# Kernel optimization log

Measured on AMD Instinct MI355X. Metric: run time of the kernel, lower is better.

The kernel has to match this reference:

```python
import jax, jax.numpy as jnp
import numpy as np

MODEL_DIM = 2048
NUM_HEADS = 32
HEAD_DIM = 64
NUM_KV_HEADS = 8
ROPE_BASE = 10000.0
BATCH = 2
SEQ = 2048


def setup_inputs() -> dict:
    key = jax.random.key(0)
    ks = jax.random.split(key, 5)
    sd = 1.0 / np.sqrt(MODEL_DIM)
    x = jax.random.normal(ks[0], (BATCH, SEQ, MODEL_DIM), dtype=jnp.float32)
    Wq = jax.random.normal(ks[1], (MODEL_DIM, NUM_HEADS * HEAD_DIM), dtype=jnp.float32) * sd
    Wk = jax.random.normal(ks[2], (MODEL_DIM, NUM_KV_HEADS * HEAD_DIM), dtype=jnp.float32) * sd
    Wv = jax.random.normal(ks[3], (MODEL_DIM, NUM_KV_HEADS * HEAD_DIM), dtype=jnp.float32) * sd
    Wo = jax.random.normal(ks[4], (NUM_HEADS * HEAD_DIM, MODEL_DIM), dtype=jnp.float32) * sd
    return {"x": x, "Wq": Wq, "Wk": Wk, "Wv": Wv, "Wo": Wo}


def _rope_cache(seq_len, head_dim, base, dtype):
    # inv_freq over even dims, standard rotate-half (Llama-style) RoPE cache
    inv_freq = 1.0 / (base ** (jnp.arange(0, head_dim, 2, dtype=jnp.float32) / head_dim))
    t = jnp.arange(seq_len, dtype=jnp.float32)
    freqs = jnp.outer(t, inv_freq)               # [S, hd/2]
    emb = jnp.concatenate([freqs, freqs], axis=-1)  # [S, hd]
    return jnp.cos(emb).astype(dtype), jnp.sin(emb).astype(dtype)


def _rotate_half(x):
    h = x.shape[-1] // 2
    return jnp.concatenate([-x[..., h:], x[..., :h]], axis=-1)


def _apply_rope(q, k, cos, sin):
    # q,k: [B, H, S, hd]; cos,sin: [S, hd] -> broadcast over batch/heads
    cos = cos[None, None, :, :]
    sin = sin[None, None, :, :]
    q = q * cos + _rotate_half(q) * sin
    k = k * cos + _rotate_half(k) * sin
    return q, k


def reference(x, Wq, Wk, Wv, Wo):
    bsz, seq_len, _ = x.shape
    q_per_kv = NUM_HEADS // NUM_KV_HEADS

    # projections -> [B, H, S, hd]
    q = (x @ Wq).reshape(bsz, seq_len, NUM_HEADS, HEAD_DIM).transpose(0, 2, 1, 3)
    k = (x @ Wk).reshape(bsz, seq_len, NUM_KV_HEADS, HEAD_DIM).transpose(0, 2, 1, 3)
    v = (x @ Wv).reshape(bsz, seq_len, NUM_KV_HEADS, HEAD_DIM).transpose(0, 2, 1, 3)

    # GQA: repeat_interleave KV heads to match Q heads
    k = jnp.repeat(k, q_per_kv, axis=1)
    v = jnp.repeat(v, q_per_kv, axis=1)

    cos, sin = _rope_cache(seq_len, HEAD_DIM, ROPE_BASE, x.dtype)
    q, k = _apply_rope(q, k, cos, sin)

    scale = 1.0 / np.sqrt(HEAD_DIM)
    scores = jnp.einsum('bhqd,bhkd->bhqk', q, k) * scale  # [B,H,S,S]
    causal = jnp.tril(jnp.ones((seq_len, seq_len), dtype=bool))
    scores = jnp.where(causal[None, None], scores, jnp.finfo(scores.dtype).min)
    attn = jax.nn.softmax(scores, axis=-1)
    y = jnp.einsum('bhqk,bhkd->bhqd', attn, v)  # [B,H,S,hd]

    y = y.transpose(0, 2, 1, 3).reshape(bsz, seq_len, NUM_HEADS * HEAD_DIM)
    return y @ Wo
```

## Files before the change

kernel.cpp:

```cpp
#include <hip/hip_runtime.h>
#include <cstdint>

typedef unsigned short u16;
typedef __attribute__((ext_vector_type(8))) short short8;
typedef __attribute__((ext_vector_type(4))) short short4v;
typedef __attribute__((ext_vector_type(4))) float f32x4;

#define SEQ     2048
#define NHEADS  32
#define NKV     8
#define HD      64
#define DM      2048
#define MROWS   4096
#define KVSTR   1024
#define PSTR    88

__device__ __forceinline__ float b2f(unsigned int u) {
    return __builtin_bit_cast(float, u << 16);
}
__device__ __forceinline__ u16 f2b(float f) {
    unsigned int u = __builtin_bit_cast(unsigned int, f);
    return (u16)((u + 0x7fffu + ((u >> 16) & 1u)) >> 16);
}

__device__ __forceinline__ float dpp_red_max16(float x) {
    int v = __builtin_bit_cast(int, x);
    x = fmaxf(x, __builtin_bit_cast(float,
        __builtin_amdgcn_update_dpp(v, v, 0xB1, 0xF, 0xF, true)));
    v = __builtin_bit_cast(int, x);
    x = fmaxf(x, __builtin_bit_cast(float,
        __builtin_amdgcn_update_dpp(v, v, 0x4E, 0xF, 0xF, true)));
    v = __builtin_bit_cast(int, x);
    x = fmaxf(x, __builtin_bit_cast(float,
        __builtin_amdgcn_update_dpp(v, v, 0x141, 0xF, 0xF, true)));
    v = __builtin_bit_cast(int, x);
    x = fmaxf(x, __builtin_bit_cast(float,
        __builtin_amdgcn_update_dpp(v, v, 0x140, 0xF, 0xF, true)));
    return x;
}
__device__ __forceinline__ float dpp_red_sum16(float x) {
    int v = __builtin_bit_cast(int, x);
    x = x + __builtin_bit_cast(float,
        __builtin_amdgcn_update_dpp(v, v, 0xB1, 0xF, 0xF, true));
    v = __builtin_bit_cast(int, x);
    x = x + __builtin_bit_cast(float,
        __builtin_amdgcn_update_dpp(v, v, 0x4E, 0xF, 0xF, true));
    v = __builtin_bit_cast(int, x);
    x = x + __builtin_bit_cast(float,
        __builtin_amdgcn_update_dpp(v, v, 0x141, 0xF, 0xF, true));
    v = __builtin_bit_cast(int, x);
    x = x + __builtin_bit_cast(float,
        __builtin_amdgcn_update_dpp(v, v, 0x140, 0xF, 0xF, true));
    return x;
}

#define GLOAD_LDS16(g, l)                                              \
    __builtin_amdgcn_global_load_lds(                                  \
        (const __attribute__((address_space(1))) void*)(g),            \
        (__attribute__((address_space(3))) void*)(l), 16, 0, 0)

__global__ __launch_bounds__(256) void cvt_f32_bf16(
    const float* __restrict__ in, u16* __restrict__ out, int n4) {
    int i = blockIdx.x * 256 + threadIdx.x;
    if (i < n4) {
        float4 v = ((const float4*)in)[i];
        ushort4 o;
        o.x = f2b(v.x); o.y = f2b(v.y); o.z = f2b(v.z); o.w = f2b(v.w);
        ((ushort4*)out)[i] = o;
    }
}

__global__ __launch_bounds__(256) void rope_table_kernel(
    float* __restrict__ cosT, float* __restrict__ sinT) {
    int idx = blockIdx.x * 256 + threadIdx.x;
    int s  = idx >> 5;
    int dl = idx & 31;
    float inv_freq = exp2f((float)dl * -0.41524101186092025f);
    float ang = (float)s * inv_freq;
    float sn, cs;
    sincosf(ang, &sn, &cs);
    cosT[idx] = cs;
    sinT[idx] = sn;
}

__global__ __launch_bounds__(256) void transpose_f32_bf16(
    const float* __restrict__ in, u16* __restrict__ out, int K, int N) {
    __shared__ float tile[32][33];
    int n0 = blockIdx.x * 32, k0 = blockIdx.y * 32;
    int tx = threadIdx.x, ty = threadIdx.y;
    for (int r = ty; r < 32; r += 8)
        tile[r][tx] = in[(size_t)(k0 + r) * N + n0 + tx];
    __syncthreads();
    for (int r = ty; r < 32; r += 8)
        out[(size_t)(n0 + r) * K + k0 + tx] = f2b(tile[tx][r]);
}

#define GEMM_BODY(Aptr, BTptr, Kdim)                                        \
    __shared__ __align__(16) u16 rA[3][4096];                               \
    __shared__ __align__(16) u16 rB[3][4096];                               \
    const int tid  = threadIdx.x;                                           \
    const int wid  = tid >> 6;                                              \
    const int lane = tid & 63;                                              \
    const int quad = lane >> 4;                                             \
    const int l16  = lane & 15;                                             \
    const int nwg  = gridDim.x * gridDim.y;                                 \
    const int fid  = blockIdx.y * gridDim.x + blockIdx.x;                   \
    const int swz  = (fid & 7) * (nwg >> 3) + (fid >> 3);                   \
    const int rowBase = (swz / gridDim.x) * 128;                            \
    const int colBase = (swz % gridDim.x) * 128;                            \
    const int wr = (wid >> 1) * 64;                                         \
    const int wc = (wid & 1) * 64;                                          \
    size_t sAoff[2], sBoff[2];                                              \
    int ldOff[2];                                                           \
    _Pragma("unroll")                                                       \
    for (int j = 0; j < 2; ++j) {                                           \
        const int p = j * 256 + tid;       \
        const int q = p >> 3;                                               \
        const int u = (p & 7) ^ (q & 7);               \
        const int r = (q << 1) | (u >> 2);                                  \
        const int sc = (u & 3) * 8;              \
        sAoff[j] = (size_t)(rowBase + r) * (Kdim) + sc;                     \
        sBoff[j] = (size_t)(colBase + r) * (Kdim) + sc;                     \
        ldOff[j] = (j * 256 + (wid << 6)) * 8;    \
    }                                                                       \
    int aOff[4], bOff[4];                  \
    _Pragma("unroll")                                                       \
    for (int mi = 0; mi < 4; ++mi) {                                        \
        const int ra = wr + mi * 16 + l16;                                  \
        const int qa = ra >> 1;                                             \
        const int ua = ((ra & 1) << 2) | quad;                              \
        aOff[mi] = (qa * 8 + (ua ^ (qa & 7))) * 8;                          \
        const int rb = wc + mi * 16 + l16;                                  \
        const int qb = rb >> 1;                                             \
        const int ub = ((rb & 1) << 2) | quad;                              \
        bOff[mi] = (qb * 8 + (ub ^ (qb & 7))) * 8;                          \
    }                                                                       \
    f32x4 acc[4][4] = {};                                                   \
    const int NT = (Kdim) / 32;                                             \
    _Pragma("unroll")                                                       \
    for (int st = 0; st < 3; ++st) {       \
        _Pragma("unroll")                                                   \
        for (int j = 0; j < 2; ++j) {                                       \
            GLOAD_LDS16(Aptr  + sAoff[j] + st * 32, &rA[st][ldOff[j]]);     \
            GLOAD_LDS16(BTptr + sBoff[j] + st * 32, &rB[st][ldOff[j]]);     \
        }                                                                   \
    }                                                                       \
    int bs = 0;                            \
    for (int s = 0; s < NT; ++s) {                                          \
        if (s < NT - 1)                                                     \
            asm volatile("s_waitcnt vmcnt(4)\n\ts_barrier" ::: "memory");   \
        else                                                                \
            asm volatile("s_waitcnt vmcnt(0)\n\ts_barrier" ::: "memory");   \
        const u16* Ab = rA[bs];                                             \
        const u16* Bb = rB[bs];                                             \
        short8 a[4], b[4];                                                  \
        _Pragma("unroll")                                                   \
        for (int mi = 0; mi < 4; ++mi) a[mi] = *(const short8*)&Ab[aOff[mi]]; \
        _Pragma("unroll")                                                   \
        for (int ni = 0; ni < 4; ++ni) b[ni] = *(const short8*)&Bb[bOff[ni]]; \
        if (s + 2 < NT) {                           \
            const int bi = bs == 0 ? 2 : bs - 1;               \
            const int kk = (s + 2) * 32;                                    \
            _Pragma("unroll")                                               \
            for (int j = 0; j < 2; ++j) {                                   \
                GLOAD_LDS16(Aptr  + sAoff[j] + kk, &rA[bi][ldOff[j]]);      \
                GLOAD_LDS16(BTptr + sBoff[j] + kk, &rB[bi][ldOff[j]]);      \
            }                                                               \
        }                                                                   \
        __builtin_amdgcn_s_setprio(1);                                      \
        _Pragma("unroll")                                                   \
        for (int mi = 0; mi < 4; ++mi)                                      \
            _Pragma("unroll")                                               \
            for (int ni = 0; ni < 4; ++ni)                                  \
                acc[mi][ni] = __builtin_amdgcn_mfma_f32_16x16x32_bf16(      \
                    a[mi], b[ni], acc[mi][ni], 0, 0, 0);                    \
        __builtin_amdgcn_s_setprio(0);                                      \
        bs = bs == 2 ? 0 : bs + 1;                                          \
    }                                                                       \
    const int wRow = rowBase + wr;                                          \
    const int wCol = colBase + wc;

__global__ __launch_bounds__(256, 3) void gemm_qkv(
    const u16* __restrict__ A, const u16* __restrict__ BT,
    u16* __restrict__ Qb, u16* __restrict__ KVb,
    const float* __restrict__ cosT, const float* __restrict__ sinT) {
    GEMM_BODY(A, BT, DM)

    u16* dst;
    int dstride, dcol;
    float scale;
    bool doRope;
    if (wCol < 2048)      { dst = Qb;  dstride = 2048; dcol = wCol;        scale = 0.125f; doRope = true;  }
    else if (wCol < 2560) { dst = KVb; dstride = 1024; dcol = wCol - 2048; scale = 1.0f;   doRope = true;  }
    else                  { dst = KVb; dstride = 1024; dcol = wCol - 2048; scale = 1.0f;   doRope = false; }

#pragma unroll
    for (int mi = 0; mi < 4; ++mi) {
#pragma unroll
        for (int r = 0; r < 4; ++r) {
            const int R = wRow + mi * 16 + quad * 4 + r;
            u16* crow = dst + (size_t)R * dstride + dcol;
            if (doRope) {
                const int s = R & (SEQ - 1);
#pragma unroll
                for (int ni = 0; ni < 2; ++ni) {
                    const int dl = ni * 16 + l16;
                    float lo = acc[mi][ni][r];
                    float hi = acc[mi][ni + 2][r];
                    float cs = cosT[s * 32 + dl];
                    float sn = sinT[s * 32 + dl];
                    crow[dl]      = f2b((lo * cs - hi * sn) * scale);
                    crow[dl + 32] = f2b((hi * cs + lo * sn) * scale);
                }
            } else {
#pragma unroll
                for (int ni = 0; ni < 4; ++ni)
                    crow[ni * 16 + l16] = f2b(acc[mi][ni][r]);
            }
        }
    }
}

__global__ __launch_bounds__(256, 3) void gemm_out(
    const u16* __restrict__ A, const u16* __restrict__ BT,
    float* __restrict__ C32) {
    GEMM_BODY(A, BT, DM)
#pragma unroll
    for (int mi = 0; mi < 4; ++mi) {
#pragma unroll
        for (int r = 0; r < 4; ++r) {
            const int R = wRow + mi * 16 + quad * 4 + r;
            float* crow = C32 + (size_t)R * DM + wCol;
#pragma unroll
            for (int ni = 0; ni < 4; ++ni)
                crow[ni * 16 + l16] = acc[mi][ni][r];
        }
    }
}

__global__ __launch_bounds__(512, 4) void flash_attn(
    const u16* __restrict__ Q, const u16* __restrict__ KV,
    u16* __restrict__ Yb, float* __restrict__ PoA,
    float* __restrict__ Ml) {
    __shared__ __align__(16) u16 Ks[64 * 64];
    __shared__ __align__(16) u16 Vt[64 * 72];
    __shared__ __align__(16) u16 Ps[8 * 16 * PSTR];

    const int p   = blockIdx.x >> 1;
    const int sh  = blockIdx.x & 1;
    const int h   = blockIdx.y;
    const int b   = blockIdx.z;
    const int kvh = h >> 2;
    const int tid  = threadIdx.x;
    const int wid  = tid >> 6;
    const int lane = tid & 63;
    const int quad = lane >> 4;
    const int l16  = lane & 15;

    const u16* Kg = KV + (size_t)b * SEQ * KVSTR + kvh * HD;
    const u16* Vg = Kg + 512;
    u16* Psw = Ps + wid * 16 * PSTR;

    const int kKey = tid >> 3, kCc = tid & 7;
    const int vkp  = tid & 31;
    const int vd0  = (tid >> 5) * 4;

    for (int ph = 0; ph < 2; ++ph) {
        const int qt = ph ? (15 - p) : p;
        const int hc = ph ? (16 - p) : (p + 1);
        const int tS = sh * hc;
        const int rowBaseW = qt * 128 + wid * 16;

        short8 qf[2];
#pragma unroll
        for (int ks = 0; ks < 2; ++ks)
            qf[ks] = *(const short8*)&Q[
                (size_t)(b * SEQ + rowBaseW + l16) * (NHEADS * HD)
                + h * HD + ks * 32 + quad * 8];

        f32x4 o[4] = {};
        float mi[4], li[4];
#pragma unroll
        for (int r = 0; r < 4; ++r) { mi[r] = -3e38f; li[r] = 0.f; }

        const size_t jF = (size_t)tS * 64;
        short8  kreg = *(const short8*)&Kg[(jF + kKey) * KVSTR + kCc * 8];
        short4v vrA  = *(const short4v*)&Vg[(jF + 2 * vkp)     * KVSTR + vd0];
        short4v vrB  = *(const short4v*)&Vg[(jF + 2 * vkp + 1) * KVSTR + vd0];

        for (int tt = 0; tt < hc; ++tt) {
            const int j0 = (tS + tt) * 64;
            __syncthreads();

            *(short8*)&Ks[kKey * 64 + ((kCc ^ (kKey & 7)) * 8)] = kreg;
#pragma unroll
            for (int i = 0; i < 4; ++i) {
                unsigned int w = (unsigned int)(u16)vrA[i]
                               | ((unsigned int)(u16)vrB[i] << 16);
                ((unsigned int*)Vt)[(vd0 + i) * 36 + vkp] = w;
            }
            __syncthreads();

            if (tt + 1 < hc) {
                const size_t jn = (size_t)(j0 + 64);
                kreg = *(const short8*)&Kg[(jn + kKey) * KVSTR + kCc * 8];
                vrA  = *(const short4v*)&Vg[(jn + 2 * vkp)     * KVSTR + vd0];
                vrB  = *(const short4v*)&Vg[(jn + 2 * vkp + 1) * KVSTR + vd0];
            }

            f32x4 s[4] = {};
#pragma unroll
            for (int ks = 0; ks < 2; ++ks)
#pragma unroll
                for (int ct = 0; ct < 4; ++ct) {
                    int key = ct * 16 + l16;
                    int cc  = (ks * 4 + quad) ^ (key & 7);
                    short8 bk = *(const short8*)&Ks[key * 64 + cc * 8];
                    s[ct] = __builtin_amdgcn_mfma_f32_16x16x32_bf16(
                        qf[ks], bk, s[ct], 0, 0, 0);
                }

            if (j0 + 63 > rowBaseW) {
#pragma unroll
                for (int ct = 0; ct < 4; ++ct)
#pragma unroll
                    for (int r = 0; r < 4; ++r) {
                        int R = rowBaseW + quad * 4 + r;
                        int J = j0 + ct * 16 + l16;
                        if (J > R) s[ct][r] = -3e38f;
                    }
            }

#pragma unroll
            for (int r = 0; r < 4; ++r) {
                float rmax = fmaxf(fmaxf(s[0][r], s[1][r]),
                                   fmaxf(s[2][r], s[3][r]));
                rmax = dpp_red_max16(rmax);
                float mnew  = fmaxf(mi[r], rmax);
                float alpha = __expf(mi[r] - mnew);
                mi[r] = mnew;
                float rs = 0.f;
#pragma unroll
                for (int ct = 0; ct < 4; ++ct) {
                    float pv = __expf(s[ct][r] - mnew);
                    s[ct][r] = pv;
                    rs += pv;
                    o[ct][r] *= alpha;
                }
                rs = dpp_red_sum16(rs);
                li[r] = li[r] * alpha + rs;
            }

#pragma unroll
            for (int ct = 0; ct < 4; ++ct)
#pragma unroll
                for (int r = 0; r < 4; ++r)
                    Psw[(quad * 4 + r) * PSTR + ct * 16 + l16] = f2b(s[ct][r]);

            short8 pa[2];
#pragma unroll
            for (int ks = 0; ks < 2; ++ks)
                pa[ks] = *(const short8*)&Psw[l16 * PSTR + ks * 32 + quad * 8];
#pragma unroll
            for (int ks = 0; ks < 2; ++ks)
#pragma unroll
                for (int ct = 0; ct < 4; ++ct) {
                    short8 vbf = *(const short8*)&Vt[(ct * 16 + l16) * 72 + ks * 32 + quad * 8];
                    o[ct] = __builtin_amdgcn_mfma_f32_16x16x32_bf16(
                        pa[ks], vbf, o[ct], 0, 0, 0);
                }
        }

        float rli[4];
#pragma unroll
        for (int r = 0; r < 4; ++r)
            rli[r] = li[r] > 0.f ? 1.0f / li[r] : 0.f;
        if (sh == 0) {
#pragma unroll
            for (int r = 0; r < 4; ++r) {
                int R = rowBaseW + quad * 4 + r;
                float* arow = PoA + (size_t)(b * SEQ + R) * (NHEADS * HD) + h * HD;
#pragma unroll
                for (int ct = 0; ct < 4; ++ct)
                    arow[ct * 16 + l16] = o[ct][r] * rli[r];
            }
        } else {
#pragma unroll
            for (int r = 0; r < 4; ++r) {
                int R = rowBaseW + quad * 4 + r;
                u16* yrow = Yb + (size_t)(b * SEQ + R) * (NHEADS * HD) + h * HD;
#pragma unroll
                for (int ct = 0; ct < 4; ++ct)
                    yrow[ct * 16 + l16] = f2b(o[ct][r] * rli[r]);
            }
        }
        if (l16 == 0) {
            float2* MlX = (float2*)Ml + (size_t)sh * 131072
                        + ((b * 32 + h) * 2048 + rowBaseW + quad * 4);
#pragma unroll
            for (int r = 0; r < 4; ++r)
                MlX[r] = make_float2(mi[r], li[r]);
        }
    }
}

__global__ __launch_bounds__(256) void combine_kernel(
    const float* __restrict__ PoA, const float* __restrict__ Ml,
    u16* __restrict__ Yb) {
    const size_t e = ((size_t)blockIdx.x * 256 + threadIdx.x) * 8;
    const int rowg = (int)(e >> 11);
    const int c    = (int)(e & 2047);
    const int h    = c >> 6;
    const int bz   = rowg >> 11;
    const int row  = rowg & 2047;
    const int slot = ((bz * 32 + h) * 2048 + row) * 2;
    const float mA = Ml[slot],          lA = Ml[slot + 1];
    const float mB = Ml[262144 + slot], lB = Ml[262144 + slot + 1];
    const float m  = fmaxf(mA, mB);
    const float wA = lA * __expf(mA - m);
    const float wB = lB * __expf(mB - m);
    const float inv = 1.0f / (wA + wB);
    const float a = wA * inv, bw = wB * inv;
    float4 A0 = *(const float4*)(PoA + e);
    float4 A1 = *(const float4*)(PoA + e + 4);
    short8 Bv = *(const short8*)(Yb + e);
    float av[8] = {A0.x, A0.y, A0.z, A0.w, A1.x, A1.y, A1.z, A1.w};
    u16 yo[8];
#pragma unroll
    for (int j = 0; j < 8; ++j)
        yo[j] = f2b(a * av[j] + bw * b2f((unsigned int)(u16)Bv[j]));
    *(short8*)(Yb + e) = *(short8*)yo;
}

extern "C" void kernel_launch(void* const* d_in, const int* in_sizes, int n_in,
                              void* d_out, int out_size, void* d_ws, size_t ws_size,
                              hipStream_t stream) {
    const float* x  = (const float*)d_in[0];
    const float* Wq = (const float*)d_in[1];
    const float* Wk = (const float*)d_in[2];
    const float* Wv = (const float*)d_in[3];
    const float* Wo = (const float*)d_in[4];
    float* out = (float*)d_out;

    char* ws = (char*)d_ws;
    u16*  xb    = (u16*)(ws);
    u16*  WqkvT = (u16*)(ws + 16777216);
    u16*  WoT   = (u16*)(ws + 29360128);
    u16*  Qb    = (u16*)(ws + 37748736);
    u16*  KVb   = (u16*)(ws + 54525952);
    u16*  Yb    = (u16*)(ws + 62914560);
    float* cosT = (float*)(ws + 79691776);
    float* sinT = (float*)(ws + 79953920);
    float* PoA  = (float*)(ws);
    float* Ml   = (float*)(ws + 33554432);

    rope_table_kernel<<<dim3(65536 / 256), 256, 0, stream>>>(cosT, sinT);

    cvt_f32_bf16<<<dim3(MROWS * DM / 4 / 256), 256, 0, stream>>>(x, xb, MROWS * DM / 4);

    dim3 tb(32, 8);
    transpose_f32_bf16<<<dim3(2048/32, 2048/32), tb, 0, stream>>>(Wq, WqkvT, 2048, 2048);
    transpose_f32_bf16<<<dim3( 512/32, 2048/32), tb, 0, stream>>>(Wk, WqkvT + 2048 * 2048, 2048, 512);
    transpose_f32_bf16<<<dim3( 512/32, 2048/32), tb, 0, stream>>>(Wv, WqkvT + 2560 * 2048, 2048, 512);

    gemm_qkv<<<dim3(24, 32), 256, 0, stream>>>(xb, WqkvT, Qb, KVb, cosT, sinT);

    flash_attn<<<dim3(16, NHEADS, 2), 512, 0, stream>>>(Qb, KVb, Yb, PoA, Ml);

    combine_kernel<<<dim3(4096), 256, 0, stream>>>(PoA, Ml, Yb);

    transpose_f32_bf16<<<dim3(2048/32, 2048/32), tb, 0, stream>>>(Wo, WoT, 2048, 2048);

    gemm_out<<<dim3(16, 32), 256, 0, stream>>>(Yb, WoT, out);
}
```

Baseline: 342.4 us.

## Give each attention wave two 16-row query tiles and rescale online softmax lazily

The flash-attention kernel now runs 4 waves per block instead of 8. Each wave handles 32 query rows as two 16-row tiles, so every K and V fragment read from LDS feeds two MFMAs. The softmax rescale of the output and running sum is skipped unless the row max grows by more than a threshold, which cuts exp and multiply work per tile. The GEMM prologue also stops issuing a redundant third-stage load. The cost is more registers per thread, fewer waves to hide latency, and more global K/V loads per thread.

New measurement: 344.2 us. About the same (+0.5%).

```diff
diff --git a/kernel.cpp b/kernel.cpp
--- a/kernel.cpp
+++ b/kernel.cpp
@@ -138,7 +138,7 @@
     f32x4 acc[4][4] = {};                                                   \
     const int NT = (Kdim) / 32;                                             \
     _Pragma("unroll")                                                       \
-    for (int st = 0; st < 3; ++st) {       \
+    for (int st = 0; st < 2; ++st) {         \
         _Pragma("unroll")                                                   \
         for (int j = 0; j < 2; ++j) {                                       \
             GLOAD_LDS16(Aptr  + sAoff[j] + st * 32, &rA[st][ldOff[j]]);     \
@@ -158,7 +158,7 @@
         for (int mi = 0; mi < 4; ++mi) a[mi] = *(const short8*)&Ab[aOff[mi]]; \
         _Pragma("unroll")                                                   \
         for (int ni = 0; ni < 4; ++ni) b[ni] = *(const short8*)&Bb[bOff[ni]]; \
-        if (s + 2 < NT) {                           \
+        if (s + 2 < NT) {                    \
             const int bi = bs == 0 ? 2 : bs - 1;               \
             const int kk = (s + 2) * 32;                                    \
             _Pragma("unroll")                                               \
@@ -238,13 +238,13 @@
     }
 }
 
-__global__ __launch_bounds__(512, 4) void flash_attn(
+__global__ __launch_bounds__(256, 3) void flash_attn(
     const u16* __restrict__ Q, const u16* __restrict__ KV,
     u16* __restrict__ Yb, float* __restrict__ PoA,
     float* __restrict__ Ml) {
     __shared__ __align__(16) u16 Ks[64 * 64];
     __shared__ __align__(16) u16 Vt[64 * 72];
-    __shared__ __align__(16) u16 Ps[8 * 16 * PSTR];
+    __shared__ __align__(16) u16 Ps[4 * 32 * PSTR];
 
     const int p   = blockIdx.x >> 1;
     const int sh  = blockIdx.x & 1;
@@ -259,56 +259,62 @@
 
     const u16* Kg = KV + (size_t)b * SEQ * KVSTR + kvh * HD;
     const u16* Vg = Kg + 512;
-    u16* Psw = Ps + wid * 16 * PSTR;
-
-    const int kKey = tid >> 3, kCc = tid & 7;
+    u16* Psw = Ps + wid * 32 * PSTR;
+
+    const int kKey = tid >> 2;
+    const int kC0  = (tid & 3) * 2;
     const int vkp  = tid & 31;
-    const int vd0  = (tid >> 5) * 4;
+    const int vd0  = (tid >> 5) * 8;
 
     for (int ph = 0; ph < 2; ++ph) {
         const int qt = ph ? (15 - p) : p;
         const int hc = ph ? (16 - p) : (p + 1);
         const int tS = sh * hc;
-        const int rowBaseW = qt * 128 + wid * 16;
-
-        short8 qf[2];
-#pragma unroll
-        for (int ks = 0; ks < 2; ++ks)
-            qf[ks] = *(const short8*)&Q[
-                (size_t)(b * SEQ + rowBaseW + l16) * (NHEADS * HD)
-                + h * HD + ks * 32 + quad * 8];
-
-        f32x4 o[4] = {};
-        float mi[4], li[4];
-#pragma unroll
-        for (int r = 0; r < 4; ++r) { mi[r] = -3e38f; li[r] = 0.f; }
+        const int rowBaseW = qt * 128 + wid * 32;
+
+        short8 qf[2][2];
+#pragma unroll
+        for (int rt = 0; rt < 2; ++rt)
+#pragma unroll
+            for (int ks = 0; ks < 2; ++ks)
+                qf[rt][ks] = *(const short8*)&Q[
+                    (size_t)(b * SEQ + rowBaseW + rt * 16 + l16) * (NHEADS * HD)
+                    + h * HD + ks * 32 + quad * 8];
+
+        f32x4 o[2][4] = {};
+        float mi[8], li[8];
+#pragma unroll
+        for (int i = 0; i < 8; ++i) { mi[i] = -3e38f; li[i] = 0.f; }
 
         const size_t jF = (size_t)tS * 64;
-        short8  kreg = *(const short8*)&Kg[(jF + kKey) * KVSTR + kCc * 8];
-        short4v vrA  = *(const short4v*)&Vg[(jF + 2 * vkp)     * KVSTR + vd0];
-        short4v vrB  = *(const short4v*)&Vg[(jF + 2 * vkp + 1) * KVSTR + vd0];
+        short8 kreg0 = *(const short8*)&Kg[(jF + kKey) * KVSTR + kC0 * 8];
+        short8 kreg1 = *(const short8*)&Kg[(jF + kKey) * KVSTR + kC0 * 8 + 8];
+        short8 vA = *(const short8*)&Vg[(jF + 2 * vkp)     * KVSTR + vd0];
+        short8 vB = *(const short8*)&Vg[(jF + 2 * vkp + 1) * KVSTR + vd0];
 
         for (int tt = 0; tt < hc; ++tt) {
             const int j0 = (tS + tt) * 64;
             __syncthreads();
 
-            *(short8*)&Ks[kKey * 64 + ((kCc ^ (kKey & 7)) * 8)] = kreg;
-#pragma unroll
-            for (int i = 0; i < 4; ++i) {
-                unsigned int w = (unsigned int)(u16)vrA[i]
-                               | ((unsigned int)(u16)vrB[i] << 16);
+            *(short8*)&Ks[kKey * 64 + (((kC0)     ^ (kKey & 7)) * 8)] = kreg0;
+            *(short8*)&Ks[kKey * 64 + (((kC0 + 1) ^ (kKey & 7)) * 8)] = kreg1;
+#pragma unroll
+            for (int i = 0; i < 8; ++i) {
+                unsigned int w = (unsigned int)(u16)vA[i]
+                               | ((unsigned int)(u16)vB[i] << 16);
                 ((unsigned int*)Vt)[(vd0 + i) * 36 + vkp] = w;
             }
             __syncthreads();
 
             if (tt + 1 < hc) {
                 const size_t jn = (size_t)(j0 + 64);
-                kreg = *(const short8*)&Kg[(jn + kKey) * KVSTR + kCc * 8];
-                vrA  = *(const short4v*)&Vg[(jn + 2 * vkp)     * KVSTR + vd0];
-                vrB  = *(const short4v*)&Vg[(jn + 2 * vkp + 1) * KVSTR + vd0];
+                kreg0 = *(const short8*)&Kg[(jn + kKey) * KVSTR + kC0 * 8];
+                kreg1 = *(const short8*)&Kg[(jn + kKey) * KVSTR + kC0 * 8 + 8];
+                vA = *(const short8*)&Vg[(jn + 2 * vkp)     * KVSTR + vd0];
+                vB = *(const short8*)&Vg[(jn + 2 * vkp + 1) * KVSTR + vd0];
             }
 
-            f32x4 s[4] = {};
+            f32x4 s[2][4] = {};
 #pragma unroll
             for (int ks = 0; ks < 2; ++ks)
 #pragma unroll
@@ -316,90 +322,113 @@
                     int key = ct * 16 + l16;
                     int cc  = (ks * 4 + quad) ^ (key & 7);
                     short8 bk = *(const short8*)&Ks[key * 64 + cc * 8];
-                    s[ct] = __builtin_amdgcn_mfma_f32_16x16x32_bf16(
-                        qf[ks], bk, s[ct], 0, 0, 0);
-                }
-
-            if (j0 + 63 > rowBaseW) {
+                    s[0][ct] = __builtin_amdgcn_mfma_f32_16x16x32_bf16(
+                        qf[0][ks], bk, s[0][ct], 0, 0, 0);
+                    s[1][ct] = __builtin_amdgcn_mfma_f32_16x16x32_bf16(
+                        qf[1][ks], bk, s[1][ct], 0, 0, 0);
+                }
+
+#pragma unroll
+            for (int rt = 0; rt < 2; ++rt) {
+                const int rB = rowBaseW + rt * 16;
+                if (j0 + 63 > rB) {
+#pragma unroll
+                    for (int ct = 0; ct < 4; ++ct)
+#pragma unroll
+                        for (int r = 0; r < 4; ++r) {
+                            int R = rB + quad * 4 + r;
+                            int J = j0 + ct * 16 + l16;
+                            if (J > R) s[rt][ct][r] = -3e38f;
+                        }
+                }
+            }
+
+#pragma unroll
+            for (int rt = 0; rt < 2; ++rt)
+#pragma unroll
+                for (int r = 0; r < 4; ++r) {
+                    const int ix = rt * 4 + r;
+                    float rmax = fmaxf(fmaxf(s[rt][0][r], s[rt][1][r]),
+                                       fmaxf(s[rt][2][r], s[rt][3][r]));
+                    rmax = dpp_red_max16(rmax);
+                    if (!__all(rmax <= mi[ix] + 8.f)) {
+                        float mnew  = fmaxf(mi[ix], rmax);
+                        float alpha = __expf(mi[ix] - mnew);
+                        mi[ix] = mnew;
+                        li[ix] *= alpha;
+#pragma unroll
+                        for (int ct = 0; ct < 4; ++ct) o[rt][ct][r] *= alpha;
+                    }
+                    float rs = 0.f;
+#pragma unroll
+                    for (int ct = 0; ct < 4; ++ct) {
+                        float pv = __expf(s[rt][ct][r] - mi[ix]);
+                        s[rt][ct][r] = pv;
+                        rs += pv;
+                    }
+                    rs = dpp_red_sum16(rs);
+                    li[ix] += rs;
+                }
+
+#pragma unroll
+            for (int rt = 0; rt < 2; ++rt)
 #pragma unroll
                 for (int ct = 0; ct < 4; ++ct)
 #pragma unroll
-                    for (int r = 0; r < 4; ++r) {
-                        int R = rowBaseW + quad * 4 + r;
-                        int J = j0 + ct * 16 + l16;
-                        if (J > R) s[ct][r] = -3e38f;
-                    }
-            }
-
-#pragma unroll
-            for (int r = 0; r < 4; ++r) {
-                float rmax = fmaxf(fmaxf(s[0][r], s[1][r]),
-                                   fmaxf(s[2][r], s[3][r]));
-                rmax = dpp_red_max16(rmax);
-                float mnew  = fmaxf(mi[r], rmax);
-                float alpha = __expf(mi[r] - mnew);
-                mi[r] = mnew;
-                float rs = 0.f;
-#pragma unroll
-                for (int ct = 0; ct < 4; ++ct) {
-                    float pv = __expf(s[ct][r] - mnew);
-                    s[ct][r] = pv;
-                    rs += pv;
-                    o[ct][r] *= alpha;
-                }
-                rs = dpp_red_sum16(rs);
-                li[r] = li[r] * alpha + rs;
-            }
-
-#pragma unroll
-            for (int ct = 0; ct < 4; ++ct)
-#pragma unroll
-                for (int r = 0; r < 4; ++r)
-                    Psw[(quad * 4 + r) * PSTR + ct * 16 + l16] = f2b(s[ct][r]);
-
-            short8 pa[2];
-#pragma unroll
-            for (int ks = 0; ks < 2; ++ks)
-                pa[ks] = *(const short8*)&Psw[l16 * PSTR + ks * 32 + quad * 8];
-#pragma unroll
-            for (int ks = 0; ks < 2; ++ks)
+                    for (int r = 0; r < 4; ++r)
+                        Psw[(rt * 16 + quad * 4 + r) * PSTR + ct * 16 + l16]
+                            = f2b(s[rt][ct][r]);
+
+#pragma unroll
+            for (int ks = 0; ks < 2; ++ks) {
+                short8 pa0 = *(const short8*)&Psw[l16 * PSTR + ks * 32 + quad * 8];
+                short8 pa1 = *(const short8*)&Psw[(16 + l16) * PSTR + ks * 32 + quad * 8];
 #pragma unroll
                 for (int ct = 0; ct < 4; ++ct) {
                     short8 vbf = *(const short8*)&Vt[(ct * 16 + l16) * 72 + ks * 32 + quad * 8];
-                    o[ct] = __builtin_amdgcn_mfma_f32_16x16x32_bf16(
-                        pa[ks], vbf, o[ct], 0, 0, 0);
-                }
+                    o[0][ct] = __builtin_amdgcn_mfma_f32_16x16x32_bf16(
+                        pa0, vbf, o[0][ct], 0, 0, 0);
+                    o[1][ct] = __builtin_amdgcn_mfma_f32_16x16x32_bf16(
+                        pa1, vbf, o[1][ct], 0, 0, 0);
+                }
+            }
         }
 
-        float rli[4];
-#pragma unroll
-        for (int r = 0; r < 4; ++r)
-            rli[r] = li[r] > 0.f ? 1.0f / li[r] : 0.f;
+        float rli[8];
+#pragma unroll
+        for (int i = 0; i < 8; ++i)
+            rli[i] = li[i] > 0.f ? 1.0f / li[i] : 0.f;
         if (sh == 0) {
 #pragma unroll
-            for (int r = 0; r < 4; ++r) {
-                int R = rowBaseW + quad * 4 + r;
-                float* arow = PoA + (size_t)(b * SEQ + R) * (NHEADS * HD) + h * HD;
-#pragma unroll
-                for (int ct = 0; ct < 4; ++ct)
-                    arow[ct * 16 + l16] = o[ct][r] * rli[r];
-            }
+            for (int rt = 0; rt < 2; ++rt)
+#pragma unroll
+                for (int r = 0; r < 4; ++r) {
+                    int R = rowBaseW + rt * 16 + quad * 4 + r;
+                    float* arow = PoA + (size_t)(b * SEQ + R) * (NHEADS * HD) + h * HD;
+#pragma unroll
+                    for (int ct = 0; ct < 4; ++ct)
+                        arow[ct * 16 + l16] = o[rt][ct][r] * rli[rt * 4 + r];
+                }
         } else {
 #pragma unroll
-            for (int r = 0; r < 4; ++r) {
-                int R = rowBaseW + quad * 4 + r;
-                u16* yrow = Yb + (size_t)(b * SEQ + R) * (NHEADS * HD) + h * HD;
-#pragma unroll
-                for (int ct = 0; ct < 4; ++ct)
-                    yrow[ct * 16 + l16] = f2b(o[ct][r] * rli[r]);
-            }
+            for (int rt = 0; rt < 2; ++rt)
+#pragma unroll
+                for (int r = 0; r < 4; ++r) {
+                    int R = rowBaseW + rt * 16 + quad * 4 + r;
+                    u16* yrow = Yb + (size_t)(b * SEQ + R) * (NHEADS * HD) + h * HD;
+#pragma unroll
+                    for (int ct = 0; ct < 4; ++ct)
+                        yrow[ct * 16 + l16] = f2b(o[rt][ct][r] * rli[rt * 4 + r]);
+                }
         }
         if (l16 == 0) {
             float2* MlX = (float2*)Ml + (size_t)sh * 131072
                         + ((b * 32 + h) * 2048 + rowBaseW + quad * 4);
 #pragma unroll
-            for (int r = 0; r < 4; ++r)
-                MlX[r] = make_float2(mi[r], li[r]);
+            for (int rt = 0; rt < 2; ++rt)
+#pragma unroll
+                for (int r = 0; r < 4; ++r)
+                    MlX[rt * 16 + r] = make_float2(mi[rt * 4 + r], li[rt * 4 + r]);
         }
     }
 }
@@ -465,7 +494,7 @@
 
     gemm_qkv<<<dim3(24, 32), 256, 0, stream>>>(xb, WqkvT, Qb, KVb, cosT, sinT);
 
-    flash_attn<<<dim3(16, NHEADS, 2), 512, 0, stream>>>(Qb, KVb, Yb, PoA, Ml);
+    flash_attn<<<dim3(16, NHEADS, 2), 256, 0, stream>>>(Qb, KVb, Yb, PoA, Ml);
 
     combine_kernel<<<dim3(4096), 256, 0, stream>>>(PoA, Ml, Yb);
 
```
